# Optimization experiments

Hardware: AMD Instinct MI355X
Metric: run time of the kernel (lower is better)

Reference implementation:

```python
import jax, jax.numpy as jnp
import numpy as np

G, N, E = 4, 50000, 800000
F_IN, HID, OUT = 64, 128, 64


def setup_inputs() -> dict:
    key = jax.random.key(0)
    ks = jax.random.split(key, 4)
    x = jax.random.normal(ks[0], (G, N, F_IN), dtype=jnp.float32)
    edge_index = jax.random.randint(ks[1], (G, 2, E), 0, N)
    W1 = jax.random.normal(ks[2], (G, F_IN, HID), dtype=jnp.float32) / np.sqrt(F_IN).astype(np.float32)
    b1 = jnp.zeros((G, HID), dtype=jnp.float32)
    W2 = jax.random.normal(ks[3], (G, HID, OUT), dtype=jnp.float32) / np.sqrt(HID).astype(np.float32)
    b2 = jnp.zeros((G, OUT), dtype=jnp.float32)
    return {"x": x, "edge_index": edge_index, "W1": W1, "b1": b1, "W2": W2, "b2": b2}


def gcn_conv(x, src, dst, W, b):
    # PyG GCNConv: add self loops, symmetric norm D^-1/2 (A+I) D^-1/2, then XW + b
    n = x.shape[0]
    loop = jnp.arange(n)
    s = jnp.concatenate([src, loop])  # [E+N]
    d = jnp.concatenate([dst, loop])
    deg = jax.ops.segment_sum(jnp.ones_like(s, dtype=x.dtype), d, num_segments=n)
    dinv = jax.lax.rsqrt(deg)  # deg >= 1 because of self loops
    norm = dinv[s] * dinv[d]  # [E+N]
    h = x @ W  # [N, F_out]
    msg = h[s] * norm[:, None]  # edge-wise gather (memory-bound)
    out = jax.ops.segment_sum(msg, d, num_segments=n)  # scatter-add
    return out + b


def reference(x, edge_index, W1, b1, W2, b2):
    def per_graph(xg, eg, w1, b1g, w2, b2g):
        src, dst = eg[0], eg[1]
        h = jax.nn.elu(gcn_conv(xg, src, dst, w1, b1g))
        h = jax.nn.elu(gcn_conv(h, src, dst, w2, b2g))
        return h  # [N, OUT]

    out = jax.vmap(per_graph)(x, edge_index, W1, b1, W2, b2)  # [G, N, OUT]
    return out.reshape(G * N, OUT)  # torch.cat over graphs along dim 0
```

## Files before the change

kernel.cpp:

```cpp
#include <hip/hip_runtime.h>
#include <cstdint>

constexpr int G = 4, N = 50000, E = 800000;
constexpr int FIN = 64, HID = 128, FOUT = 64;
constexpr int NB = (N + 1023) / 1024;

constexpr int PB = 64;
constexpr int CP = E / PB;
constexpr int NBK = (N + 255) / 256;

constexpr int NT = (N + 63) / 64;
constexpr int NTH = 391;

typedef unsigned short ushort;
typedef _Float16 f16;

__device__ __forceinline__ ushort f2h(float f) {
  f16 h = (f16)f;
  return __builtin_bit_cast(ushort, h);
}
__device__ __forceinline__ float h2f(ushort u) {
  f16 h = __builtin_bit_cast(f16, u);
  return (float)h;
}

__device__ __forceinline__ void xcd_map(int b, int& g, int& chunk) {
  int xcd = b & 7;
  int sub = b >> 3;
  g = xcd >> 1;
  chunk = (xcd & 1) * 6250 + sub;
}

__global__ void k_x2h(const float4* __restrict__ X, const float* __restrict__ dinv,
                      ushort4* __restrict__ Xh, int n4) {
  int i = blockIdx.x * blockDim.x + threadIdx.x;
  if (i >= n4) return;
  float sc = dinv[i >> 4];
  float4 v = X[i];
  ushort4 o = {f2h(sc * v.x), f2h(sc * v.y), f2h(sc * v.z), f2h(sc * v.w)};
  Xh[i] = o;
}


__global__ __launch_bounds__(256) void k_phist(const int* __restrict__ ei,
                                               int* __restrict__ PH) {
  __shared__ int h[NBK];
  int pb = blockIdx.x, g = blockIdx.y;
  for (int i = threadIdx.x; i < NBK; i += 256) h[i] = 0;
  __syncthreads();
  const int4* dst4 = (const int4*)(ei + (size_t)g * 2 * E + E + (size_t)pb * CP);
  for (int i = threadIdx.x; i < CP / 4; i += 256) {
    int4 d = dst4[i];
    atomicAdd(&h[d.x >> 8], 1);
    atomicAdd(&h[d.y >> 8], 1);
    atomicAdd(&h[d.z >> 8], 1);
    atomicAdd(&h[d.w >> 8], 1);
  }
  __syncthreads();
  for (int i = threadIdx.x; i < NBK; i += 256)
    PH[((size_t)g * NBK + i) * PB + pb] = h[i];
}

__global__ void k_pscan(const int* __restrict__ PH, int* __restrict__ POFF,
                        int* __restrict__ BB) {
  int g = blockIdx.x, k = threadIdx.x;
  int tot = 0;
  if (k < NBK) {
#pragma unroll 8
    for (int pb = 0; pb < PB; ++pb) tot += PH[((size_t)g * NBK + k) * PB + pb];
  }
  __shared__ int sm[256];
  sm[k] = tot;
  __syncthreads();
  for (int off = 1; off < 256; off <<= 1) {
    int v = (k >= off) ? sm[k - off] : 0;
    __syncthreads();
    sm[k] += v;
    __syncthreads();
  }
  int excl = sm[k] - tot;
  if (k < NBK) {
    BB[g * (NBK + 1) + k] = excl;
    if (k == NBK - 1) BB[g * (NBK + 1) + NBK] = excl + tot;
    int run = excl;
#pragma unroll 8
    for (int pb = 0; pb < PB; ++pb) {
      POFF[((size_t)g * NBK + k) * PB + pb] = run;
      run += PH[((size_t)g * NBK + k) * PB + pb];
    }
  }
}

__global__ __launch_bounds__(256) void k_part(const int* __restrict__ ei,
                                              const int* __restrict__ POFF,
                                              unsigned* __restrict__ pairs) {
  __shared__ int off[NBK];
  __shared__ int rk[NBK];
  int pb = blockIdx.x, g = blockIdx.y;
  for (int i = threadIdx.x; i < NBK; i += 256) {
    off[i] = POFF[((size_t)g * NBK + i) * PB + pb];
    rk[i] = 0;
  }
  __syncthreads();
  const int* base = ei + (size_t)g * 2 * E + (size_t)pb * CP;
  const int4* s4 = (const int4*)base;
  const int4* d4 = (const int4*)(base + E);
  unsigned* pg = pairs + (size_t)g * E;
  for (int i = threadIdx.x; i < CP / 4; i += 256) {
    int4 s = s4[i], d = d4[i];
    int sv[4] = {s.x, s.y, s.z, s.w};
    int dv[4] = {d.x, d.y, d.z, d.w};
#pragma unroll
    for (int k = 0; k < 4; ++k) {
      int b = dv[k] >> 8;
      int r = atomicAdd(&rk[b], 1);
      pg[off[b] + r] = (unsigned)sv[k] | ((unsigned)(dv[k] & 255) << 16);
    }
  }
}

__global__ __launch_bounds__(256) void k_bcnt(const unsigned* __restrict__ pairs,
                                              const int* __restrict__ BB,
                                              int* __restrict__ cnt) {
  __shared__ int h[256];
  int k = blockIdx.x, g = blockIdx.y;
  h[threadIdx.x] = 0;
  __syncthreads();
  int lo = BB[g * (NBK + 1) + k], hi = BB[g * (NBK + 1) + k + 1];
  const unsigned* pg = pairs + (size_t)g * E;
  for (int i = lo + (int)threadIdx.x; i < hi; i += 256)
    atomicAdd(&h[(pg[i] >> 16) & 255], 1);
  __syncthreads();
  int n0 = k << 8;
  int nn = min(256, N - n0);
  if ((int)threadIdx.x < nn) cnt[g * N + n0 + threadIdx.x] = h[threadIdx.x];
}

__global__ __launch_bounds__(256) void k_place(const unsigned* __restrict__ pairs,
                                               const int* __restrict__ BB,
                                               const int* __restrict__ rowptr,
                                               int* __restrict__ col) {
  __shared__ int rp[256];
  __shared__ int rk[256];
  int k = blockIdx.x, g = blockIdx.y;
  int n0 = k << 8;
  int nn = min(256, N - n0);
  if ((int)threadIdx.x < nn) rp[threadIdx.x] = rowptr[g * (N + 1) + n0 + threadIdx.x];
  rk[threadIdx.x] = 0;
  __syncthreads();
  int lo = BB[g * (NBK + 1) + k], hi = BB[g * (NBK + 1) + k + 1];
  const unsigned* pg = pairs + (size_t)g * E;
  int* cg = col + (size_t)g * E;
  for (int i = lo + (int)threadIdx.x; i < hi; i += 256) {
    unsigned p = pg[i];
    int dl = (p >> 16) & 255;
    int r = atomicAdd(&rk[dl], 1);
    cg[rp[dl] + r] = (int)(p & 0xffffu);
  }
}

__global__ void k_scan_partial(const int* __restrict__ cnt, int* __restrict__ part) {
  int g = blockIdx.y, b = blockIdx.x, tid = threadIdx.x;
  int base = b * 1024 + tid * 4;
  int s = 0;
#pragma unroll
  for (int k = 0; k < 4; ++k) {
    int i = base + k;
    if (i < N) s += cnt[g * N + i];
  }
  __shared__ int sm[256];
  sm[tid] = s;
  __syncthreads();
  for (int off = 128; off > 0; off >>= 1) {
    if (tid < off) sm[tid] += sm[tid + off];
    __syncthreads();
  }
  if (tid == 0) part[g * NB + b] = sm[0];
}

__global__ void k_scan_mid(int* __restrict__ part, int* __restrict__ rowptr) {
  int g = blockIdx.x;
  if (threadIdx.x != 0) return;
  int run = 0;
  for (int b = 0; b < NB; ++b) {
    int t = part[g * NB + b];
    part[g * NB + b] = run;
    run += t;
  }
  rowptr[g * (N + 1) + N] = run;
}

__global__ void k_scan_final(const int* __restrict__ cnt, const int* __restrict__ part,
                             int* __restrict__ rowptr, float* __restrict__ dinv) {
  int g = blockIdx.y, b = blockIdx.x, tid = threadIdx.x;
  int base = b * 1024 + tid * 4;
  int c[4];
  int s = 0;
#pragma unroll
  for (int k = 0; k < 4; ++k) {
    int i = base + k;
    c[k] = (i < N) ? cnt[g * N + i] : 0;
    s += c[k];
  }
  __shared__ int sm[256];
  sm[tid] = s;
  __syncthreads();
  for (int off = 1; off < 256; off <<= 1) {
    int v = (tid >= off) ? sm[tid - off] : 0;
    __syncthreads();
    sm[tid] += v;
    __syncthreads();
  }
  int excl = sm[tid] - s + part[g * NB + b];
#pragma unroll
  for (int k = 0; k < 4; ++k) {
    int i = base + k;
    if (i < N) {
      rowptr[g * (N + 1) + i] = excl;
      dinv[g * N + i] = rsqrtf((float)(c[k] + 1));
    }
    excl += c[k];
  }
}

__device__ __forceinline__ float agg_row(const ushort* __restrict__ hb,
                                         const int* __restrict__ cl, int rs, int re,
                                         int lane, float acc) {
  int j = rs;
  for (; j + 16 <= re; j += 16) {
    int s[16];
#pragma unroll
    for (int k = 0; k < 16; ++k) s[k] = cl[j + k];
    float v[16];
#pragma unroll
    for (int k = 0; k < 16; ++k) v[k] = h2f(hb[(size_t)s[k] * 64 + lane]);
#pragma unroll
    for (int k = 0; k < 16; ++k) acc += v[k];
  }
  for (; j + 8 <= re; j += 8) {
    int s[8];
#pragma unroll
    for (int k = 0; k < 8; ++k) s[k] = cl[j + k];
    float v[8];
#pragma unroll
    for (int k = 0; k < 8; ++k) v[k] = h2f(hb[(size_t)s[k] * 64 + lane]);
#pragma unroll
    for (int k = 0; k < 8; ++k) acc += v[k];
  }
  for (; j < re; ++j) acc += h2f(hb[(size_t)cl[j] * 64 + lane]);
  return acc;
}

__global__ __launch_bounds__(256) void k_l1(const ushort* __restrict__ Xh,
                                            const int* __restrict__ rowptr,
                                            const int* __restrict__ col,
                                            const float* __restrict__ dinv,
                                            const float* __restrict__ W1,
                                            const float* __restrict__ b1,
                                            const float* __restrict__ W2,
                                            ushort* __restrict__ H2s) {
  constexpr int PK = FIN + 1;
  __shared__ float lds[64 * PK];
  ushort* h1s = (ushort*)lds;
  int b = blockIdx.x;
  int xcd = b & 7;
  int sub = b >> 3;
  int g = xcd >> 1;
  int tile = (xcd & 1) * NTH + sub;
  int R0 = tile * 64;
  int wv = threadIdx.x >> 6;
  int lane = threadIdx.x & 63;
  const ushort* hb = Xh + (size_t)g * N * FIN;
  const int* cl = col + (size_t)g * E;
  for (int i = 0; i < 16; ++i) {
    int d = __builtin_amdgcn_readfirstlane(R0 + wv * 16 + i);
    float zv = 0.f;
    if (d < N) {
      int rs = rowptr[g * (N + 1) + d];
      int re = rowptr[g * (N + 1) + d + 1];
      float acc = h2f(hb[(size_t)d * FIN + lane]);
      acc = agg_row(hb, cl, rs, re, lane, acc);
      zv = dinv[g * N + d] * acc;
    }
    lds[(wv * 16 + i) * PK + lane] = zv;
  }
  __syncthreads();
  int c0 = __builtin_amdgcn_readfirstlane(wv * 32);
  const float* W1g = W1 + (size_t)g * FIN * HID;
  const float* xrow = &lds[lane * PK];
  float acc[32];
#pragma unroll
  for (int c = 0; c < 32; ++c) acc[c] = 0.f;
#pragma unroll 4
  for (int k = 0; k < FIN; ++k) {
    float xv = xrow[k];
#pragma unroll
    for (int c = 0; c < 32; ++c)
      acc[c] = fmaf(xv, W1g[(size_t)k * HID + c0 + c], acc[c]);
  }
#pragma unroll
  for (int c = 0; c < 32; ++c) {
    float v = acc[c] + b1[g * HID + c0 + c];
    acc[c] = v > 0.f ? v : expm1f(v);
  }
  __syncthreads();
#pragma unroll
  for (int c2 = 0; c2 < 16; ++c2) {
    unsigned pk = (unsigned)f2h(acc[2 * c2]) | ((unsigned)f2h(acc[2 * c2 + 1]) << 16);
    *(unsigned*)&h1s[lane * 130 + c0 + 2 * c2] = pk;
  }
  __syncthreads();
  int j0 = __builtin_amdgcn_readfirstlane(wv * 16);
  const float* W2g = W2 + (size_t)g * HID * FOUT + j0;
  float acc2[16];
#pragma unroll
  for (int j = 0; j < 16; ++j) acc2[j] = 0.f;
#pragma unroll 4
  for (int c = 0; c < HID; c += 2) {
    unsigned pk = *(const unsigned*)&h1s[lane * 130 + c];
    float f0 = h2f((ushort)(pk & 0xffffu));
    float f1 = h2f((ushort)(pk >> 16));
    const float* w0 = &W2g[(size_t)c * FOUT];
    const float* w1 = &W2g[(size_t)(c + 1) * FOUT];
#pragma unroll
    for (int j = 0; j < 16; ++j) acc2[j] = fmaf(f0, w0[j], acc2[j]);
#pragma unroll
    for (int j = 0; j < 16; ++j) acc2[j] = fmaf(f1, w1[j], acc2[j]);
  }
  int row = R0 + lane;
  if (row < N) {
    float dd = dinv[g * N + row];
    ushort o[16];
#pragma unroll
    for (int j = 0; j < 16; ++j) o[j] = f2h(acc2[j] * dd);
    ushort* dst = H2s + ((size_t)g * N + row) * FOUT + j0;
    *(uint4*)dst = *(uint4*)&o[0];
    *(uint4*)(dst + 8) = *(uint4*)&o[8];
  }
}

template <int F>
__global__ __launch_bounds__(256) void k_agg_out(const ushort* __restrict__ Hsrc,
                                                 const int* __restrict__ rowptr,
                                                 const int* __restrict__ col,
                                                 const float* __restrict__ dinv,
                                                 const float* __restrict__ bias,
                                                 float* __restrict__ out) {
  int g, chunk;
  xcd_map(blockIdx.x, g, chunk);
  int d = __builtin_amdgcn_readfirstlane(chunk * 4 + (threadIdx.x >> 6));
  int lane = threadIdx.x & 63;
  const ushort* hb = Hsrc + (size_t)g * N * F;
  const int* cl = col + (size_t)g * E;
  int rs = rowptr[g * (N + 1) + d];
  int re = rowptr[g * (N + 1) + d + 1];
  float acc = h2f(hb[(size_t)d * F + lane]);
  acc = agg_row(hb, cl, rs, re, lane, acc);
  float p = acc * dinv[g * N + d] + bias[g * F + lane];
  p = p > 0.f ? p : expm1f(p);
  out[((size_t)g * N + d) * F + lane] = p;
}

extern "C" void kernel_launch(void* const* d_in, const int* in_sizes, int n_in,
                              void* d_out, int out_size, void* d_ws, size_t ws_size,
                              hipStream_t stream) {
  const float* x = (const float*)d_in[0];
  const int* ei = (const int*)d_in[1];
  const float* W1 = (const float*)d_in[2];
  const float* b1 = (const float*)d_in[3];
  const float* W2 = (const float*)d_in[4];
  const float* b2 = (const float*)d_in[5];
  float* out = (float*)d_out;

  char* p = (char*)d_ws;
  auto alloc = [&](size_t bytes) {
    char* r = p;
    p += (bytes + 255) & ~(size_t)255;
    return r;
  };
  int* cnt = (int*)alloc(sizeof(int) * G * N);
  int* rowptr = (int*)alloc(sizeof(int) * G * (N + 1));
  int* part = (int*)alloc(sizeof(int) * G * NB);
  float* dinv = (float*)alloc(sizeof(float) * G * N);
  int* col = (int*)alloc(sizeof(int) * (size_t)G * E);
  float* z = (float*)alloc(sizeof(float) * (size_t)G * N * FIN);
  char* scratch = (char*)alloc((size_t)103 << 20);
  ushort* h2s = (ushort*)z;
  unsigned* pairs = (unsigned*)scratch;
  int* PH = (int*)(scratch + ((size_t)13 << 20));
  int* POFF = (int*)(scratch + ((size_t)14 << 20));
  int* BB = (int*)(scratch + ((size_t)15 << 20));
  ushort* xh = (ushort*)(scratch + ((size_t)32 << 20));

  k_phist<<<dim3(PB, G), 256, 0, stream>>>(ei, PH);
  k_pscan<<<G, 256, 0, stream>>>(PH, POFF, BB);
  k_part<<<dim3(PB, G), 256, 0, stream>>>(ei, POFF, pairs);
  k_bcnt<<<dim3(NBK, G), 256, 0, stream>>>(pairs, BB, cnt);
  dim3 sg(NB, G);
  k_scan_partial<<<sg, 256, 0, stream>>>(cnt, part);
  k_scan_mid<<<G, 64, 0, stream>>>(part, rowptr);
  k_scan_final<<<sg, 256, 0, stream>>>(cnt, part, rowptr, dinv);
  k_place<<<dim3(NBK, G), 256, 0, stream>>>(pairs, BB, rowptr, col);

  k_x2h<<<(G * N * FIN / 4 + 255) / 256, 256, 0, stream>>>(
      (const float4*)x, dinv, (ushort4*)xh, G * N * FIN / 4);

  k_l1<<<8 * NTH, 256, 0, stream>>>(xh, rowptr, col, dinv, W1, b1, W2, h2s);

  k_agg_out<FOUT><<<(G * N) / 4, 256, 0, stream>>>(h2s, rowptr, col, dinv, b2, out);
}
```

Measured before the change: 445.5 us.

## Use MFMA f16 matrix cores for fused layer-1 and W2 transforms

Replaces the scalar FMA dense transforms in the fused layer-1 kernel with 16x16x32 f16 MFMA instructions, staging aggregated rows and hidden activations in LDS as f16. A new small kernel pre-packs W1 and W2 into f16 fragment layout so each lane loads its B operand as one vector. This targets the ALU-bound matmul portion of k_l1, at the cost of rounding aggregated features and weights to f16 and an extra launch. Output stores become scalar 2-byte writes per lane instead of 16-byte vector stores.

```diff
diff --git a/kernel.cpp b/kernel.cpp
--- a/kernel.cpp
+++ b/kernel.cpp
@@ -14,6 +14,8 @@
 
 typedef unsigned short ushort;
 typedef _Float16 f16;
+typedef _Float16 h8 __attribute__((ext_vector_type(8)));
+typedef float f4 __attribute__((ext_vector_type(4)));
 
 __device__ __forceinline__ ushort f2h(float f) {
   f16 h = (f16)f;
@@ -41,6 +43,27 @@
   Xh[i] = o;
 }
 
+__global__ void k_wprep(const float* __restrict__ W1, const float* __restrict__ W2,
+                        ushort* __restrict__ W1f, ushort* __restrict__ W2f) {
+  int g = blockIdx.x;
+  int l = threadIdx.x;
+  for (int nt = 0; nt < 8; ++nt)
+    for (int kb = 0; kb < 2; ++kb)
+      for (int j = 0; j < 8; ++j) {
+        int k = kb * 32 + (l >> 4) * 8 + j;
+        int n = nt * 16 + (l & 15);
+        W1f[((((size_t)g * 8 + nt) * 2 + kb) * 64 + l) * 8 + j] =
+            f2h(W1[((size_t)g * FIN + k) * HID + n]);
+      }
+  for (int nt = 0; nt < 4; ++nt)
+    for (int kb = 0; kb < 4; ++kb)
+      for (int j = 0; j < 8; ++j) {
+        int k = kb * 32 + (l >> 4) * 8 + j;
+        int n = nt * 16 + (l & 15);
+        W2f[((((size_t)g * 4 + nt) * 4 + kb) * 64 + l) * 8 + j] =
+            f2h(W2[((size_t)g * HID + k) * FOUT + n]);
+      }
+}
 
 __global__ __launch_bounds__(256) void k_phist(const int* __restrict__ ei,
                                                int* __restrict__ PH) {
@@ -255,13 +278,13 @@
                                             const int* __restrict__ rowptr,
                                             const int* __restrict__ col,
                                             const float* __restrict__ dinv,
-                                            const float* __restrict__ W1,
+                                            const ushort* __restrict__ W1f,
                                             const float* __restrict__ b1,
-                                            const float* __restrict__ W2,
+                                            const ushort* __restrict__ W2f,
                                             ushort* __restrict__ H2s) {
-  constexpr int PK = FIN + 1;
-  __shared__ float lds[64 * PK];
-  ushort* h1s = (ushort*)lds;
+  constexpr int PZ = 72;
+  constexpr int PH1 = 136;
+  __shared__ alignas(16) ushort sm[64 * PH1];
   int b = blockIdx.x;
   int xcd = b & 7;
   int sub = b >> 3;
@@ -270,6 +293,7 @@
   int R0 = tile * 64;
   int wv = threadIdx.x >> 6;
   int lane = threadIdx.x & 63;
+  int l4 = lane >> 4, l15 = lane & 15;
   const ushort* hb = Xh + (size_t)g * N * FIN;
   const int* cl = col + (size_t)g * E;
   for (int i = 0; i < 16; ++i) {
@@ -282,60 +306,75 @@
       acc = agg_row(hb, cl, rs, re, lane, acc);
       zv = dinv[g * N + d] * acc;
     }
-    lds[(wv * 16 + i) * PK + lane] = zv;
-  }
-  __syncthreads();
-  int c0 = __builtin_amdgcn_readfirstlane(wv * 32);
-  const float* W1g = W1 + (size_t)g * FIN * HID;
-  const float* xrow = &lds[lane * PK];
-  float acc[32];
-#pragma unroll
-  for (int c = 0; c < 32; ++c) acc[c] = 0.f;
-#pragma unroll 4
-  for (int k = 0; k < FIN; ++k) {
-    float xv = xrow[k];
-#pragma unroll
-    for (int c = 0; c < 32; ++c)
-      acc[c] = fmaf(xv, W1g[(size_t)k * HID + c0 + c], acc[c]);
-  }
-#pragma unroll
-  for (int c = 0; c < 32; ++c) {
-    float v = acc[c] + b1[g * HID + c0 + c];
-    acc[c] = v > 0.f ? v : expm1f(v);
-  }
-  __syncthreads();
-#pragma unroll
-  for (int c2 = 0; c2 < 16; ++c2) {
-    unsigned pk = (unsigned)f2h(acc[2 * c2]) | ((unsigned)f2h(acc[2 * c2 + 1]) << 16);
-    *(unsigned*)&h1s[lane * 130 + c0 + 2 * c2] = pk;
-  }
-  __syncthreads();
-  int j0 = __builtin_amdgcn_readfirstlane(wv * 16);
-  const float* W2g = W2 + (size_t)g * HID * FOUT + j0;
-  float acc2[16];
-#pragma unroll
-  for (int j = 0; j < 16; ++j) acc2[j] = 0.f;
-#pragma unroll 4
-  for (int c = 0; c < HID; c += 2) {
-    unsigned pk = *(const unsigned*)&h1s[lane * 130 + c];
-    float f0 = h2f((ushort)(pk & 0xffffu));
-    float f1 = h2f((ushort)(pk >> 16));
-    const float* w0 = &W2g[(size_t)c * FOUT];
-    const float* w1 = &W2g[(size_t)(c + 1) * FOUT];
-#pragma unroll
-    for (int j = 0; j < 16; ++j) acc2[j] = fmaf(f0, w0[j], acc2[j]);
-#pragma unroll
-    for (int j = 0; j < 16; ++j) acc2[j] = fmaf(f1, w1[j], acc2[j]);
-  }
-  int row = R0 + lane;
-  if (row < N) {
-    float dd = dinv[g * N + row];
-    ushort o[16];
-#pragma unroll
-    for (int j = 0; j < 16; ++j) o[j] = f2h(acc2[j] * dd);
-    ushort* dst = H2s + ((size_t)g * N + row) * FOUT + j0;
-    *(uint4*)dst = *(uint4*)&o[0];
-    *(uint4*)(dst + 8) = *(uint4*)&o[8];
+    sm[(wv * 16 + i) * PZ + lane] = f2h(zv);
+  }
+  __syncthreads();
+  f4 acc1[4][2];
+#pragma unroll
+  for (int m = 0; m < 4; ++m)
+#pragma unroll
+    for (int nn = 0; nn < 2; ++nn) acc1[m][nn] = (f4){0.f, 0.f, 0.f, 0.f};
+  h8 bf1[2][2];
+#pragma unroll
+  for (int nn = 0; nn < 2; ++nn)
+#pragma unroll
+    for (int kb = 0; kb < 2; ++kb)
+      bf1[nn][kb] = *(const h8*)&W1f[((((size_t)g * 8 + (2 * wv + nn)) * 2 + kb) * 64 + lane) * 8];
+#pragma unroll
+  for (int m = 0; m < 4; ++m) {
+#pragma unroll
+    for (int kb = 0; kb < 2; ++kb) {
+      h8 af = *(const h8*)&sm[(m * 16 + l15) * PZ + kb * 32 + l4 * 8];
+#pragma unroll
+      for (int nn = 0; nn < 2; ++nn)
+        acc1[m][nn] = __builtin_amdgcn_mfma_f32_16x16x32_f16(af, bf1[nn][kb],
+                                                             acc1[m][nn], 0, 0, 0);
+    }
+  }
+  float bv[2];
+#pragma unroll
+  for (int nn = 0; nn < 2; ++nn) bv[nn] = b1[g * HID + (2 * wv + nn) * 16 + l15];
+#pragma unroll
+  for (int m = 0; m < 4; ++m)
+#pragma unroll
+    for (int nn = 0; nn < 2; ++nn)
+#pragma unroll
+      for (int r = 0; r < 4; ++r) {
+        float v = acc1[m][nn][r] + bv[nn];
+        acc1[m][nn][r] = v > 0.f ? v : expm1f(v);
+      }
+  __syncthreads();
+#pragma unroll
+  for (int m = 0; m < 4; ++m)
+#pragma unroll
+    for (int nn = 0; nn < 2; ++nn) {
+      int c = (2 * wv + nn) * 16 + l15;
+#pragma unroll
+      for (int r = 0; r < 4; ++r)
+        sm[(m * 16 + l4 * 4 + r) * PH1 + c] = f2h(acc1[m][nn][r]);
+    }
+  __syncthreads();
+  h8 bf2[4];
+#pragma unroll
+  for (int kb = 0; kb < 4; ++kb)
+    bf2[kb] = *(const h8*)&W2f[((((size_t)g * 4 + wv) * 4 + kb) * 64 + lane) * 8];
+  int colo = wv * 16 + l15;
+#pragma unroll
+  for (int m = 0; m < 4; ++m) {
+    f4 a2 = (f4){0.f, 0.f, 0.f, 0.f};
+#pragma unroll
+    for (int kb = 0; kb < 4; ++kb) {
+      h8 af = *(const h8*)&sm[(m * 16 + l15) * PH1 + kb * 32 + l4 * 8];
+      a2 = __builtin_amdgcn_mfma_f32_16x16x32_f16(af, bf2[kb], a2, 0, 0, 0);
+    }
+#pragma unroll
+    for (int r = 0; r < 4; ++r) {
+      int row = R0 + m * 16 + l4 * 4 + r;
+      if (row < N) {
+        float dd = dinv[g * N + row];
+        H2s[((size_t)g * N + row) * FOUT + colo] = f2h(a2[r] * dd);
+      }
+    }
   }
 }
 
@@ -390,7 +429,11 @@
   int* PH = (int*)(scratch + ((size_t)13 << 20));
   int* POFF = (int*)(scratch + ((size_t)14 << 20));
   int* BB = (int*)(scratch + ((size_t)15 << 20));
+  ushort* W1f = (ushort*)(scratch + ((size_t)16 << 20));
+  ushort* W2f = (ushort*)(scratch + ((size_t)17 << 20));
   ushort* xh = (ushort*)(scratch + ((size_t)32 << 20));
+
+  k_wprep<<<G, 64, 0, stream>>>(W1, W2, W1f, W2f);
 
   k_phist<<<dim3(PB, G), 256, 0, stream>>>(ei, PH);
   k_pscan<<<G, 256, 0, stream>>>(PH, POFF, BB);
@@ -405,7 +448,7 @@
   k_x2h<<<(G * N * FIN / 4 + 255) / 256, 256, 0, stream>>>(
       (const float4*)x, dinv, (ushort4*)xh, G * N * FIN / 4);
 
-  k_l1<<<8 * NTH, 256, 0, stream>>>(xh, rowptr, col, dinv, W1, b1, W2, h2s);
+  k_l1<<<8 * NTH, 256, 0, stream>>>(xh, rowptr, col, dinv, W1f, b1, W2f, h2s);
 
   k_agg_out<FOUT><<<(G * N) / 4, 256, 0, stream>>>(h2s, rowptr, col, dinv, b2, out);
 }
```

New measurement: 457.2 us. 1.03x slower.
